# Optimization experiments

Measured on AMD Instinct MI355X. Metric: run time of the kernel, lower is better.

Reference implementation:

```python
import jax, jax.numpy as jnp
import numpy as np

N_NODES = 100000
N_EDGES = 1600000
D_IN = 128
D_OUT = 128


def setup_inputs() -> dict:
    key = jax.random.key(0)
    ks = jax.random.split(key, 7)
    x = jax.random.normal(ks[0], (N_NODES, D_IN), dtype=jnp.float32)
    edge_index = jax.random.randint(ks[1], (2, N_EDGES), 0, N_NODES, dtype=jnp.int64)
    edge_weights = jax.random.uniform(ks[2], (N_EDGES,), dtype=jnp.float32)
    s = 1.0 / np.sqrt(D_IN)
    W_lin = jax.random.uniform(ks[3], (D_IN, D_OUT), minval=-s, maxval=s, dtype=jnp.float32)
    b_lin = jax.random.uniform(ks[4], (D_OUT,), minval=-s, maxval=s, dtype=jnp.float32)
    W_agg = jax.random.uniform(ks[5], (D_IN, D_OUT), minval=-s, maxval=s, dtype=jnp.float32)
    b_agg = jax.random.uniform(ks[6], (D_OUT,), minval=-s, maxval=s, dtype=jnp.float32)
    return {"x": x, "edge_index": edge_index, "edge_weights": edge_weights,
            "W_lin": W_lin, "b_lin": b_lin, "W_agg": W_agg, "b_agg": b_agg}


def reference(x, edge_index, edge_weights, W_lin, b_lin, W_agg, b_agg):
    # self transform: [N, D_out]
    self_features = x @ W_lin + b_lin
    row, col = edge_index[0], edge_index[1]
    # gather neighbor features along edges: [E, D_in]
    neighbor_features = x[col] * edge_weights[:, None]
    # per-edge transform: [E, D_out]
    msgs = neighbor_features @ W_agg + b_agg
    # scatter-add to destination nodes (index_add_ on row)
    aggregated = jax.ops.segment_sum(msgs, row, num_segments=x.shape[0])
    return self_features + aggregated
```

## Files before the change

### kernel.cpp

```cpp
#include <hip/hip_runtime.h>

#define N_NODES 100000
#define N_EDGES 1600000
#define D 128
#define SCAN_CHUNK 1024
#define NB_SCAN ((N_NODES + SCAN_CHUNK - 1) / SCAN_CHUNK)

#define BSHIFT 9
#define BUCK_NODES 512
#define NBUCK 196
#define SCAP 10240
#define PART_CHUNK 4096
#define PART_BLOCKS ((N_EDGES + PART_CHUNK - 1) / PART_CHUNK)
#define CONV_BLOCKS 6250
#define W_BLOCKS 128

typedef __attribute__((ext_vector_type(8))) short bf16x8;
typedef __attribute__((ext_vector_type(4))) float f32x4;

__device__ __forceinline__ unsigned bf16rne(float f) {
  unsigned u = __float_as_uint(f);
  return (u + 0x7fffu + ((u >> 16) & 1u)) >> 16;
}

#define T5_OFF    200
#define T5_FRAGW  100304
#define T5_SRT    116688
#define T5_XH     3316688
#define T5_ZH     9718736
#define WS_T5_BYTES ((size_t)16120784 * 4)

#define WS_OFF   100000
#define WS_BSUM  200004
#define WS_SRT   200192
#define WS_XH    3400192
#define WS_T1_BYTES ((size_t)3400192 * 4)
#define WS_T2_BYTES ((size_t)(3400192 + 6400000) * 4)

__global__ __launch_bounds__(256) void part_kernel(
    const int* __restrict__ ei, const float* __restrict__ ew,
    const float* __restrict__ x,
    const float* __restrict__ Wl, const float* __restrict__ Wa,
    int* __restrict__ pcur, int2* __restrict__ stage,
    uint4* __restrict__ xh4, unsigned short* __restrict__ fragW) {
  __shared__ int cntL[NBUCK];
  __shared__ int gbaseL[NBUCK];
  __shared__ int curL[NBUCK];
  int bid = blockIdx.x, tid = threadIdx.x;

  if (bid < PART_BLOCKS) {
    if (tid < NBUCK) cntL[tid] = 0;
    __syncthreads();
    int e0 = bid * PART_CHUNK;
#pragma unroll
    for (int k = 0; k < PART_CHUNK / 256; k++) {
      int e = e0 + k * 256 + tid;
      if (e < N_EDGES) atomicAdd(&cntL[ei[e] >> BSHIFT], 1);
    }
    __syncthreads();
    if (tid < NBUCK) {
      gbaseL[tid] = atomicAdd(&pcur[tid], cntL[tid]);
      curL[tid] = 0;
    }
    __syncthreads();
#pragma unroll
    for (int k = 0; k < PART_CHUNK / 256; k++) {
      int e = e0 + k * 256 + tid;
      if (e < N_EDGES) {
        int d = ei[e];
        int b = d >> BSHIFT;
        int s = atomicAdd(&curL[b], 1);
        stage[(size_t)b * SCAP + gbaseL[b] + s] = make_int2(
            ei[N_EDGES + e] | ((d & (BUCK_NODES - 1)) << 17), __float_as_int(ew[e]));
      }
    }
  } else if (bid < PART_BLOCKS + CONV_BLOCKS) {
    int g = (bid - PART_BLOCKS) * 256 + tid;
    const float4* xp = reinterpret_cast<const float4*>(x);
    float4 a = xp[(size_t)g * 2];
    float4 b = xp[(size_t)g * 2 + 1];
    uint4 o;
    o.x = bf16rne(a.x) | (bf16rne(a.y) << 16);
    o.y = bf16rne(a.z) | (bf16rne(a.w) << 16);
    o.z = bf16rne(b.x) | (bf16rne(b.y) << 16);
    o.w = bf16rne(b.z) | (bf16rne(b.w) << 16);
    xh4[g] = o;
  } else {
    int tau = (bid - PART_BLOCKS - CONV_BLOCKS) * 256 + tid;
    int slot = tau >> 3, j = tau & 7;
    int lane = slot & 63, ft = slot >> 6;
    int t = ft & 7, s = ft >> 3;
    int kl = (s & 3) * 32 + (lane >> 4) * 8 + j;
    int n = t * 16 + (lane & 15);
    float v = (s < 4 ? Wl : Wa)[kl * 128 + n];
    fragW[slot * 8 + j] = (unsigned short)bf16rne(v);
  }
}

__global__ __launch_bounds__(256) void binB2_kernel(const int* __restrict__ pcur,
                                                    const int2* __restrict__ stage,
                                                    int* __restrict__ off,
                                                    int2* __restrict__ srt) {
  __shared__ int pc[NBUCK];
  __shared__ int sa[BUCK_NODES];
  __shared__ int sb[BUCK_NODES];
  __shared__ int curL[BUCK_NODES];
  __shared__ int baseS, mS;
  int b = blockIdx.x, tid = threadIdx.x;
  if (tid < NBUCK) pc[tid] = pcur[tid];
  for (int i = tid; i < BUCK_NODES; i += 256) sa[i] = 0;
  __syncthreads();
  if (tid == 0) {
    int s = 0;
    for (int i = 0; i < b; i++) s += pc[i];
    baseS = s;
    mS = pc[b];
  }
  __syncthreads();
  int base = baseS, m = mS;
  const int2* sp = stage + (size_t)b * SCAP;
  for (int r = tid; r < m; r += 256)
    atomicAdd(&sa[((unsigned)sp[r].x) >> 17], 1);
  __syncthreads();
  int* srcb = sa;
  int* dstb = sb;
  for (int o = 1; o < BUCK_NODES; o <<= 1) {
    for (int p = tid; p < BUCK_NODES; p += 256)
      dstb[p] = srcb[p] + (p >= o ? srcb[p - o] : 0);
    __syncthreads();
    int* t = srcb; srcb = dstb; dstb = t;
  }
  int nb = b << BSHIFT;
  int nn = min(BUCK_NODES, N_NODES - nb);
  for (int i = tid; i < BUCK_NODES; i += 256) {
    int ex = i ? srcb[i - 1] : 0;
    curL[i] = ex;
    if (i < nn) off[nb + i] = base + ex;
  }
  if (tid == 0 && b == NBUCK - 1) off[N_NODES] = base + srcb[nn - 1];
  __syncthreads();
  for (int r = tid; r < m; r += 256) {
    int2 rec = sp[r];
    int ldst = ((unsigned)rec.x) >> 17;
    int s = atomicAdd(&curL[ldst], 1);
    srt[base + s] = make_int2(rec.x & 0x1FFFF, rec.y);
  }
}

__global__ __launch_bounds__(256) void gather_zh_kernel(const unsigned* __restrict__ xh,
                                                        const int* __restrict__ off,
                                                        const int2* __restrict__ srt,
                                                        unsigned* __restrict__ zh) {
  int gid = blockIdx.x * 256 + threadIdx.x;
  int n = gid >> 5;
  int lane = gid & 31;
  int beg = off[n], end = off[n + 1];
  float4 acc = make_float4(0.f, 0.f, 0.f, 0.f);
  int e = beg;
  for (; e + 3 < end; e += 4) {
    int2 r0 = srt[e];
    int2 r1 = srt[e + 1];
    int2 r2 = srt[e + 2];
    int2 r3 = srt[e + 3];
    uint2 p0 = *reinterpret_cast<const uint2*>(xh + (size_t)r0.x * 64 + lane * 2);
    uint2 p1 = *reinterpret_cast<const uint2*>(xh + (size_t)r1.x * 64 + lane * 2);
    uint2 p2 = *reinterpret_cast<const uint2*>(xh + (size_t)r2.x * 64 + lane * 2);
    uint2 p3 = *reinterpret_cast<const uint2*>(xh + (size_t)r3.x * 64 + lane * 2);
    float w0 = __int_as_float(r0.y), w1 = __int_as_float(r1.y);
    float w2 = __int_as_float(r2.y), w3 = __int_as_float(r3.y);
    acc.x = fmaf(w0, __uint_as_float(p0.x << 16), acc.x);
    acc.y = fmaf(w0, __uint_as_float(p0.x & 0xffff0000u), acc.y);
    acc.z = fmaf(w0, __uint_as_float(p0.y << 16), acc.z);
    acc.w = fmaf(w0, __uint_as_float(p0.y & 0xffff0000u), acc.w);
    acc.x = fmaf(w1, __uint_as_float(p1.x << 16), acc.x);
    acc.y = fmaf(w1, __uint_as_float(p1.x & 0xffff0000u), acc.y);
    acc.z = fmaf(w1, __uint_as_float(p1.y << 16), acc.z);
    acc.w = fmaf(w1, __uint_as_float(p1.y & 0xffff0000u), acc.w);
    acc.x = fmaf(w2, __uint_as_float(p2.x << 16), acc.x);
    acc.y = fmaf(w2, __uint_as_float(p2.x & 0xffff0000u), acc.y);
    acc.z = fmaf(w2, __uint_as_float(p2.y << 16), acc.z);
    acc.w = fmaf(w2, __uint_as_float(p2.y & 0xffff0000u), acc.w);
    acc.x = fmaf(w3, __uint_as_float(p3.x << 16), acc.x);
    acc.y = fmaf(w3, __uint_as_float(p3.x & 0xffff0000u), acc.y);
    acc.z = fmaf(w3, __uint_as_float(p3.y << 16), acc.z);
    acc.w = fmaf(w3, __uint_as_float(p3.y & 0xffff0000u), acc.w);
  }
  for (; e < end; e++) {
    int2 r0 = srt[e];
    uint2 p0 = *reinterpret_cast<const uint2*>(xh + (size_t)r0.x * 64 + lane * 2);
    float w0 = __int_as_float(r0.y);
    acc.x = fmaf(w0, __uint_as_float(p0.x << 16), acc.x);
    acc.y = fmaf(w0, __uint_as_float(p0.x & 0xffff0000u), acc.y);
    acc.z = fmaf(w0, __uint_as_float(p0.y << 16), acc.z);
    acc.w = fmaf(w0, __uint_as_float(p0.y & 0xffff0000u), acc.w);
  }
  uint2 o;
  o.x = bf16rne(acc.x) | (bf16rne(acc.y) << 16);
  o.y = bf16rne(acc.z) | (bf16rne(acc.w) << 16);
  *reinterpret_cast<uint2*>(zh + (size_t)n * 64 + lane * 2) = o;
}

__global__ __launch_bounds__(256) void mfma_gemm_kernel(
    const short* __restrict__ xh, const short* __restrict__ zh,
    const short* __restrict__ fragW, const int* __restrict__ off,
    const float* __restrict__ bl, const float* __restrict__ ba,
    float* __restrict__ out) {
  int tid = threadIdx.x;
  int wave = tid >> 6, lane = tid & 63;
  int m = lane & 15, q = lane >> 4;
  int R = blockIdx.x * 64 + wave * 16;
  const short* xrow = xh + (size_t)(R + m) * D + q * 8;
  const short* zrow = zh + (size_t)(R + m) * D + q * 8;
  const short* fw = fragW + (size_t)lane * 8;

  f32x4 acc[8];
#pragma unroll
  for (int t = 0; t < 8; t++) acc[t] = (f32x4){0.f, 0.f, 0.f, 0.f};

#pragma unroll
  for (int s = 0; s < 8; s++) {
    bf16x8 a = *reinterpret_cast<const bf16x8*>(s < 4 ? xrow + s * 32
                                                      : zrow + (s - 4) * 32);
#pragma unroll
    for (int t = 0; t < 8; t++) {
      bf16x8 b = *reinterpret_cast<const bf16x8*>(fw + (size_t)((s * 8 + t) * 64) * 8);
      acc[t] = __builtin_amdgcn_mfma_f32_16x16x32_bf16(a, b, acc[t], 0, 0, 0);
    }
  }

  float blv[8], bav[8];
#pragma unroll
  for (int t = 0; t < 8; t++) {
    blv[t] = bl[t * 16 + m];
    bav[t] = ba[t * 16 + m];
  }
#pragma unroll
  for (int r = 0; r < 4; r++) {
    int row = R + q * 4 + r;
    if (row < N_NODES) {
      float dg = (float)(off[row + 1] - off[row]);
#pragma unroll
      for (int t = 0; t < 8; t++)
        out[(size_t)row * D + t * 16 + m] = acc[t][r] + blv[t] + dg * bav[t];
    }
  }
}


__global__ __launch_bounds__(256) void hist_kernel(const int* __restrict__ ei,
                                                   int* __restrict__ cnt) {
  int e = blockIdx.x * 256 + threadIdx.x;
  if (e < N_EDGES) atomicAdd(&cnt[ei[e]], 1);
}

__global__ __launch_bounds__(256) void block_sum_kernel(const int* __restrict__ cnt,
                                                        int* __restrict__ bsum) {
  int base = blockIdx.x * SCAN_CHUNK;
  int s = 0;
#pragma unroll
  for (int k = 0; k < 4; k++) {
    int i = base + (int)threadIdx.x + k * 256;
    if (i < N_NODES) s += cnt[i];
  }
  __shared__ int red[4];
  for (int o = 32; o > 0; o >>= 1) s += __shfl_down(s, o, 64);
  if ((threadIdx.x & 63) == 0) red[threadIdx.x >> 6] = s;
  __syncthreads();
  if (threadIdx.x == 0) bsum[blockIdx.x] = red[0] + red[1] + red[2] + red[3];
}

__global__ __launch_bounds__(128) void scan_bsum_kernel(int* __restrict__ bsum,
                                                        int* __restrict__ off) {
  __shared__ int sh[128];
  int t = threadIdx.x;
  int v = (t < NB_SCAN) ? bsum[t] : 0;
  sh[t] = v;
  __syncthreads();
  for (int o = 1; o < 128; o <<= 1) {
    int add = (t >= o) ? sh[t - o] : 0;
    __syncthreads();
    sh[t] += add;
    __syncthreads();
  }
  if (t < NB_SCAN) bsum[t] = sh[t] - v;
  if (t == 0) off[N_NODES] = sh[127];
}

__global__ __launch_bounds__(256) void scan_offsets_kernel(const int* __restrict__ cnt,
                                                           const int* __restrict__ bsum,
                                                           int* __restrict__ off) {
  __shared__ int sh[256];
  int t = threadIdx.x;
  int i0 = blockIdx.x * SCAN_CHUNK + t * 4;
  int c[4];
#pragma unroll
  for (int k = 0; k < 4; k++) c[k] = (i0 + k < N_NODES) ? cnt[i0 + k] : 0;
  int ls = c[0] + c[1] + c[2] + c[3];
  sh[t] = ls;
  __syncthreads();
  for (int o = 1; o < 256; o <<= 1) {
    int add = (t >= o) ? sh[t - o] : 0;
    __syncthreads();
    sh[t] += add;
    __syncthreads();
  }
  int run = bsum[blockIdx.x] + sh[t] - ls;
#pragma unroll
  for (int k = 0; k < 4; k++) {
    if (i0 + k < N_NODES) off[i0 + k] = run;
    run += c[k];
  }
}

__global__ __launch_bounds__(256) void fill_kernel(const int* __restrict__ ei,
                                                   const float* __restrict__ ew,
                                                   const int* __restrict__ off,
                                                   int* __restrict__ cur,
                                                   int2* __restrict__ srt) {
  int e = blockIdx.x * 256 + threadIdx.x;
  if (e >= N_EDGES) return;
  int dst = ei[e];
  int p = off[dst] + atomicAdd(&cur[dst], 1);
  srt[p] = make_int2(ei[N_EDGES + e], __float_as_int(ew[e]));
}

__global__ __launch_bounds__(256) void convert_kernel(const float* __restrict__ x,
                                                      uint4* __restrict__ xh) {
  int i = blockIdx.x * 256 + threadIdx.x;
  const float4* xp = reinterpret_cast<const float4*>(x);
  float4 a = xp[(size_t)i * 2];
  float4 b = xp[(size_t)i * 2 + 1];
  uint4 o;
  o.x = bf16rne(a.x) | (bf16rne(a.y) << 16);
  o.y = bf16rne(a.z) | (bf16rne(a.w) << 16);
  o.z = bf16rne(b.x) | (bf16rne(b.y) << 16);
  o.w = bf16rne(b.z) | (bf16rne(b.w) << 16);
  xh[i] = o;
}

__global__ __launch_bounds__(256) void gather_bf16_kernel(const unsigned* __restrict__ xh,
                                                          const int* __restrict__ off,
                                                          const int2* __restrict__ srt,
                                                          float* __restrict__ z,
                                                          float* __restrict__ degf) {
  int gid = blockIdx.x * 256 + threadIdx.x;
  int n = gid >> 5;
  int lane = gid & 31;
  if (n >= N_NODES) return;
  int beg = off[n], end = off[n + 1];
  float4 acc = make_float4(0.f, 0.f, 0.f, 0.f);
  int e = beg;
  for (; e + 1 < end; e += 2) {
    int2 r0 = srt[e];
    int2 r1 = srt[e + 1];
    uint2 p0 = *reinterpret_cast<const uint2*>(xh + (size_t)r0.x * 64 + lane * 2);
    uint2 p1 = *reinterpret_cast<const uint2*>(xh + (size_t)r1.x * 64 + lane * 2);
    float w0 = __int_as_float(r0.y);
    float w1 = __int_as_float(r1.y);
    acc.x = fmaf(w0, __uint_as_float(p0.x << 16), acc.x);
    acc.y = fmaf(w0, __uint_as_float(p0.x & 0xffff0000u), acc.y);
    acc.z = fmaf(w0, __uint_as_float(p0.y << 16), acc.z);
    acc.w = fmaf(w0, __uint_as_float(p0.y & 0xffff0000u), acc.w);
    acc.x = fmaf(w1, __uint_as_float(p1.x << 16), acc.x);
    acc.y = fmaf(w1, __uint_as_float(p1.x & 0xffff0000u), acc.y);
    acc.z = fmaf(w1, __uint_as_float(p1.y << 16), acc.z);
    acc.w = fmaf(w1, __uint_as_float(p1.y & 0xffff0000u), acc.w);
  }
  if (e < end) {
    int2 r0 = srt[e];
    uint2 p0 = *reinterpret_cast<const uint2*>(xh + (size_t)r0.x * 64 + lane * 2);
    float w0 = __int_as_float(r0.y);
    acc.x = fmaf(w0, __uint_as_float(p0.x << 16), acc.x);
    acc.y = fmaf(w0, __uint_as_float(p0.x & 0xffff0000u), acc.y);
    acc.z = fmaf(w0, __uint_as_float(p0.y << 16), acc.z);
    acc.w = fmaf(w0, __uint_as_float(p0.y & 0xffff0000u), acc.w);
  }
  *reinterpret_cast<float4*>(z + (size_t)n * D + (lane << 2)) = acc;
  if (lane == 0) degf[n] = (float)(end - beg);
}

__global__ __launch_bounds__(256) void gather_f32_kernel(const float* __restrict__ x,
                                                         const int* __restrict__ off,
                                                         const int2* __restrict__ srt,
                                                         float* __restrict__ z,
                                                         float* __restrict__ degf) {
  int gid = blockIdx.x * 256 + threadIdx.x;
  int n = gid >> 5;
  int lane = gid & 31;
  if (n >= N_NODES) return;
  int beg = off[n], end = off[n + 1];
  float4 acc = make_float4(0.f, 0.f, 0.f, 0.f);
  for (int e = beg; e < end; e++) {
    int2 r0 = srt[e];
    float4 x0 = *reinterpret_cast<const float4*>(x + (size_t)r0.x * D + (lane << 2));
    float w0 = __int_as_float(r0.y);
    acc.x = fmaf(w0, x0.x, acc.x); acc.y = fmaf(w0, x0.y, acc.y);
    acc.z = fmaf(w0, x0.z, acc.z); acc.w = fmaf(w0, x0.w, acc.w);
  }
  *reinterpret_cast<float4*>(z + (size_t)n * D + (lane << 2)) = acc;
  if (lane == 0) degf[n] = (float)(end - beg);
}

__global__ __launch_bounds__(256) void scatter_kernel(const float* __restrict__ x,
                                                      const int* __restrict__ ei,
                                                      const float* __restrict__ ew,
                                                      float* __restrict__ z,
                                                      float* __restrict__ deg) {
  long long g = (long long)blockIdx.x * 256 + threadIdx.x;
  int e = (int)(g >> 5);
  int lane = (int)(g & 31);
  if (e >= N_EDGES) return;
  int dst = ei[e];
  int src = ei[N_EDGES + e];
  float w = ew[e];
  float4 xv = *reinterpret_cast<const float4*>(x + (size_t)src * D + (lane << 2));
  float* o = z + (size_t)dst * D + (lane << 2);
  atomicAdd(o + 0, w * xv.x);
  atomicAdd(o + 1, w * xv.y);
  atomicAdd(o + 2, w * xv.z);
  atomicAdd(o + 3, w * xv.w);
  if (lane == 0) atomicAdd(deg + dst, 1.0f);
}

__global__ __launch_bounds__(256) void fused_gemm_kernel(const float* __restrict__ x,
                                                         const float* __restrict__ Wl,
                                                         const float* __restrict__ bl,
                                                         const float* __restrict__ Wa,
                                                         const float* __restrict__ ba,
                                                         const float* __restrict__ deg,
                                                         float* __restrict__ out) {
  __shared__ float xs[32 * 16];
  __shared__ float zs[32 * 16];
  __shared__ float wls[16 * 128];
  __shared__ float was[16 * 128];
  const int tid = threadIdx.x;
  const int row0 = blockIdx.x * 32;
  const int c4 = tid & 31;
  const int r0 = tid >> 5;
  float4 acc[4];
#pragma unroll
  for (int i = 0; i < 4; i++) acc[i] = make_float4(0.f, 0.f, 0.f, 0.f);

  for (int k0 = 0; k0 < D; k0 += 16) {
    {
      int t = tid & 127;
      int r = t >> 2;
      int kc = (t & 3) << 2;
      const float* sp = (tid < 128) ? x : out;
      float* dp = (tid < 128) ? xs : zs;
      *reinterpret_cast<float4*>(dp + r * 16 + kc) =
          *reinterpret_cast<const float4*>(sp + (size_t)(row0 + r) * D + k0 + kc);
    }
#pragma unroll
    for (int i = 0; i < 2; i++) {
      int f = tid + i * 256;
      int kk = f >> 5;
      int cc = (f & 31) << 2;
      *reinterpret_cast<float4*>(wls + kk * 128 + cc) =
          *reinterpret_cast<const float4*>(Wl + (size_t)(k0 + kk) * D + cc);
      *reinterpret_cast<float4*>(was + kk * 128 + cc) =
          *reinterpret_cast<const float4*>(Wa + (size_t)(k0 + kk) * D + cc);
    }
    __syncthreads();
#pragma unroll
    for (int kk = 0; kk < 16; kk++) {
      float4 wl = *reinterpret_cast<const float4*>(wls + kk * 128 + (c4 << 2));
      float4 wa = *reinterpret_cast<const float4*>(was + kk * 128 + (c4 << 2));
#pragma unroll
      for (int rr = 0; rr < 4; rr++) {
        int r2 = r0 + rr * 8;
        float xv = xs[r2 * 16 + kk];
        float zv = zs[r2 * 16 + kk];
        acc[rr].x = fmaf(xv, wl.x, fmaf(zv, wa.x, acc[rr].x));
        acc[rr].y = fmaf(xv, wl.y, fmaf(zv, wa.y, acc[rr].y));
        acc[rr].z = fmaf(xv, wl.z, fmaf(zv, wa.z, acc[rr].z));
        acc[rr].w = fmaf(xv, wl.w, fmaf(zv, wa.w, acc[rr].w));
      }
    }
    __syncthreads();
  }

  float4 blv = *reinterpret_cast<const float4*>(bl + (c4 << 2));
  float4 bav = *reinterpret_cast<const float4*>(ba + (c4 << 2));
#pragma unroll
  for (int rr = 0; rr < 4; rr++) {
    int r = row0 + r0 + rr * 8;
    float d = deg[r];
    float4 o;
    o.x = acc[rr].x + blv.x + d * bav.x;
    o.y = acc[rr].y + blv.y + d * bav.y;
    o.z = acc[rr].z + blv.z + d * bav.z;
    o.w = acc[rr].w + blv.w + d * bav.w;
    *reinterpret_cast<float4*>(out + (size_t)r * D + (c4 << 2)) = o;
  }
}

extern "C" void kernel_launch(void* const* d_in, const int* in_sizes, int n_in,
                              void* d_out, int out_size, void* d_ws, size_t ws_size,
                              hipStream_t stream) {
  const float* x  = (const float*)d_in[0];
  const int*   ei = (const int*)d_in[1];
  const float* ew = (const float*)d_in[2];
  const float* Wl = (const float*)d_in[3];
  const float* bl = (const float*)d_in[4];
  const float* Wa = (const float*)d_in[5];
  const float* ba = (const float*)d_in[6];
  float* out = (float*)d_out;

  if (ws_size >= WS_T5_BYTES) {
    int* pcur = (int*)d_ws;
    int* off = pcur + T5_OFF;
    unsigned short* fragW = (unsigned short*)(pcur + T5_FRAGW);
    int2* srt = (int2*)(pcur + T5_SRT);
    unsigned* xh = (unsigned*)(pcur + T5_XH);
    unsigned* zh = (unsigned*)(pcur + T5_ZH);
    int2* stage = (int2*)(pcur + T5_ZH);

    hipMemsetAsync(pcur, 0, NBUCK * sizeof(int), stream);
    part_kernel<<<PART_BLOCKS + CONV_BLOCKS + W_BLOCKS, 256, 0, stream>>>(
        ei, ew, x, Wl, Wa, pcur, stage, (uint4*)xh, fragW);
    binB2_kernel<<<NBUCK, 256, 0, stream>>>(pcur, stage, off, srt);
    gather_zh_kernel<<<N_NODES * 32 / 256, 256, 0, stream>>>(xh, off, srt, zh);
    mfma_gemm_kernel<<<1563, 256, 0, stream>>>((const short*)xh, (const short*)zh,
                                               (const short*)fragW, off, bl, ba, out);
  } else if (ws_size >= WS_T1_BYTES) {
    int*  cnt  = (int*)d_ws;
    int*  off  = cnt + WS_OFF;
    int*  bsum = cnt + WS_BSUM;
    int2* srt  = (int2*)(cnt + WS_SRT);
    float* degf = (float*)cnt;

    hipMemsetAsync(cnt, 0, (size_t)N_NODES * sizeof(int), stream);
    hist_kernel<<<(N_EDGES + 255) / 256, 256, 0, stream>>>(ei, cnt);
    block_sum_kernel<<<NB_SCAN, 256, 0, stream>>>(cnt, bsum);
    scan_bsum_kernel<<<1, 128, 0, stream>>>(bsum, off);
    scan_offsets_kernel<<<NB_SCAN, 256, 0, stream>>>(cnt, bsum, off);
    hipMemsetAsync(cnt, 0, (size_t)N_NODES * sizeof(int), stream);
    fill_kernel<<<(N_EDGES + 255) / 256, 256, 0, stream>>>(ei, ew, off, cnt, srt);

    if (ws_size >= WS_T2_BYTES) {
      unsigned* xh = (unsigned*)(cnt + WS_XH);
      convert_kernel<<<(N_NODES * D / 8) / 256, 256, 0, stream>>>(x, (uint4*)xh);
      gather_bf16_kernel<<<(N_NODES * 32 + 255) / 256, 256, 0, stream>>>(xh, off, srt, out, degf);
    } else {
      gather_f32_kernel<<<(N_NODES * 32 + 255) / 256, 256, 0, stream>>>(x, off, srt, out, degf);
    }
    fused_gemm_kernel<<<N_NODES / 32, 256, 0, stream>>>(x, Wl, bl, Wa, ba, degf, out);
  } else {
    float* deg = (float*)d_ws;
    hipMemsetAsync(out, 0, (size_t)N_NODES * D * sizeof(float), stream);
    hipMemsetAsync(deg, 0, (size_t)N_NODES * sizeof(float), stream);
    scatter_kernel<<<(N_EDGES * 32) / 256, 256, 0, stream>>>(x, ei, ew, out, deg);
    fused_gemm_kernel<<<N_NODES / 32, 256, 0, stream>>>(x, Wl, bl, Wa, ba, deg, out);
  }
}
```

Before: 284.4 us.

## Add nontemporal loads/stores, widen binning block to 512, unroll gather by 8

Several streaming inputs (edge indices, weights, x for bf16 conversion, sorted edge records) are read with nontemporal loads, and the final output is written with nontemporal stores to reduce cache pollution. The bucket-sort kernel now runs 512 threads per block so each thread handles one local node in the scan. The gather kernel is unrolled to 8 edges per iteration to keep more gathers in flight. The extra unroll raises register pressure, and the nontemporal hints may not help reuse-sensitive reads.

```diff
diff --git a/kernel.cpp b/kernel.cpp
--- a/kernel.cpp
+++ b/kernel.cpp
@@ -17,6 +17,7 @@
 
 typedef __attribute__((ext_vector_type(8))) short bf16x8;
 typedef __attribute__((ext_vector_type(4))) float f32x4;
+typedef __attribute__((ext_vector_type(4))) unsigned u32x4;
 
 __device__ __forceinline__ unsigned bf16rne(float f) {
   unsigned u = __float_as_uint(f);
@@ -67,23 +68,25 @@
     for (int k = 0; k < PART_CHUNK / 256; k++) {
       int e = e0 + k * 256 + tid;
       if (e < N_EDGES) {
-        int d = ei[e];
+        int d = __builtin_nontemporal_load(ei + e);
+        int src = __builtin_nontemporal_load(ei + N_EDGES + e);
+        float w = __builtin_nontemporal_load(ew + e);
         int b = d >> BSHIFT;
         int s = atomicAdd(&curL[b], 1);
         stage[(size_t)b * SCAP + gbaseL[b] + s] = make_int2(
-            ei[N_EDGES + e] | ((d & (BUCK_NODES - 1)) << 17), __float_as_int(ew[e]));
+            src | ((d & (BUCK_NODES - 1)) << 17), __float_as_int(w));
       }
     }
   } else if (bid < PART_BLOCKS + CONV_BLOCKS) {
     int g = (bid - PART_BLOCKS) * 256 + tid;
-    const float4* xp = reinterpret_cast<const float4*>(x);
-    float4 a = xp[(size_t)g * 2];
-    float4 b = xp[(size_t)g * 2 + 1];
+    const u32x4* xp = reinterpret_cast<const u32x4*>(x);
+    u32x4 a = __builtin_nontemporal_load(xp + (size_t)g * 2);
+    u32x4 b = __builtin_nontemporal_load(xp + (size_t)g * 2 + 1);
     uint4 o;
-    o.x = bf16rne(a.x) | (bf16rne(a.y) << 16);
-    o.y = bf16rne(a.z) | (bf16rne(a.w) << 16);
-    o.z = bf16rne(b.x) | (bf16rne(b.y) << 16);
-    o.w = bf16rne(b.z) | (bf16rne(b.w) << 16);
+    o.x = bf16rne(__uint_as_float(a.x)) | (bf16rne(__uint_as_float(a.y)) << 16);
+    o.y = bf16rne(__uint_as_float(a.z)) | (bf16rne(__uint_as_float(a.w)) << 16);
+    o.z = bf16rne(__uint_as_float(b.x)) | (bf16rne(__uint_as_float(b.y)) << 16);
+    o.w = bf16rne(__uint_as_float(b.z)) | (bf16rne(__uint_as_float(b.w)) << 16);
     xh4[g] = o;
   } else {
     int tau = (bid - PART_BLOCKS - CONV_BLOCKS) * 256 + tid;
@@ -97,7 +100,7 @@
   }
 }
 
-__global__ __launch_bounds__(256) void binB2_kernel(const int* __restrict__ pcur,
+__global__ __launch_bounds__(512) void binB2_kernel(const int* __restrict__ pcur,
                                                     const int2* __restrict__ stage,
                                                     int* __restrict__ off,
                                                     int2* __restrict__ srt) {
@@ -108,7 +111,7 @@
   __shared__ int baseS, mS;
   int b = blockIdx.x, tid = threadIdx.x;
   if (tid < NBUCK) pc[tid] = pcur[tid];
-  for (int i = tid; i < BUCK_NODES; i += 256) sa[i] = 0;
+  if (tid < BUCK_NODES) sa[tid] = 0;
   __syncthreads();
   if (tid == 0) {
     int s = 0;
@@ -119,33 +122,42 @@
   __syncthreads();
   int base = baseS, m = mS;
   const int2* sp = stage + (size_t)b * SCAP;
-  for (int r = tid; r < m; r += 256)
+  for (int r = tid; r < m; r += 512)
     atomicAdd(&sa[((unsigned)sp[r].x) >> 17], 1);
   __syncthreads();
   int* srcb = sa;
   int* dstb = sb;
   for (int o = 1; o < BUCK_NODES; o <<= 1) {
-    for (int p = tid; p < BUCK_NODES; p += 256)
-      dstb[p] = srcb[p] + (p >= o ? srcb[p - o] : 0);
+    if (tid < BUCK_NODES)
+      dstb[tid] = srcb[tid] + (tid >= o ? srcb[tid - o] : 0);
     __syncthreads();
     int* t = srcb; srcb = dstb; dstb = t;
   }
   int nb = b << BSHIFT;
   int nn = min(BUCK_NODES, N_NODES - nb);
-  for (int i = tid; i < BUCK_NODES; i += 256) {
-    int ex = i ? srcb[i - 1] : 0;
-    curL[i] = ex;
-    if (i < nn) off[nb + i] = base + ex;
+  if (tid < BUCK_NODES) {
+    int ex = tid ? srcb[tid - 1] : 0;
+    curL[tid] = ex;
+    if (tid < nn) off[nb + tid] = base + ex;
   }
   if (tid == 0 && b == NBUCK - 1) off[N_NODES] = base + srcb[nn - 1];
   __syncthreads();
-  for (int r = tid; r < m; r += 256) {
+  for (int r = tid; r < m; r += 512) {
     int2 rec = sp[r];
     int ldst = ((unsigned)rec.x) >> 17;
     int s = atomicAdd(&curL[ldst], 1);
     srt[base + s] = make_int2(rec.x & 0x1FFFF, rec.y);
   }
 }
+
+#define ACC_EDGE(q_, p_)                                         \
+  {                                                              \
+    float w_ = __int_as_float((int)((q_) >> 32));                \
+    acc.x = fmaf(w_, __uint_as_float((p_).x << 16), acc.x);      \
+    acc.y = fmaf(w_, __uint_as_float((p_).x & 0xffff0000u), acc.y); \
+    acc.z = fmaf(w_, __uint_as_float((p_).y << 16), acc.z);      \
+    acc.w = fmaf(w_, __uint_as_float((p_).y & 0xffff0000u), acc.w); \
+  }
 
 __global__ __launch_bounds__(256) void gather_zh_kernel(const unsigned* __restrict__ xh,
                                                         const int* __restrict__ off,
@@ -157,42 +169,41 @@
   int beg = off[n], end = off[n + 1];
   float4 acc = make_float4(0.f, 0.f, 0.f, 0.f);
   int e = beg;
+  for (; e + 7 < end; e += 8) {
+    long long q0 = __builtin_nontemporal_load(reinterpret_cast<const long long*>(srt + e));
+    long long q1 = __builtin_nontemporal_load(reinterpret_cast<const long long*>(srt + e + 1));
+    long long q2 = __builtin_nontemporal_load(reinterpret_cast<const long long*>(srt + e + 2));
+    long long q3 = __builtin_nontemporal_load(reinterpret_cast<const long long*>(srt + e + 3));
+    long long q4 = __builtin_nontemporal_load(reinterpret_cast<const long long*>(srt + e + 4));
+    long long q5 = __builtin_nontemporal_load(reinterpret_cast<const long long*>(srt + e + 5));
+    long long q6 = __builtin_nontemporal_load(reinterpret_cast<const long long*>(srt + e + 6));
+    long long q7 = __builtin_nontemporal_load(reinterpret_cast<const long long*>(srt + e + 7));
+    uint2 p0 = *reinterpret_cast<const uint2*>(xh + (size_t)(unsigned)(q0 & 0xffffffffu) * 64 + lane * 2);
+    uint2 p1 = *reinterpret_cast<const uint2*>(xh + (size_t)(unsigned)(q1 & 0xffffffffu) * 64 + lane * 2);
+    uint2 p2 = *reinterpret_cast<const uint2*>(xh + (size_t)(unsigned)(q2 & 0xffffffffu) * 64 + lane * 2);
+    uint2 p3 = *reinterpret_cast<const uint2*>(xh + (size_t)(unsigned)(q3 & 0xffffffffu) * 64 + lane * 2);
+    uint2 p4 = *reinterpret_cast<const uint2*>(xh + (size_t)(unsigned)(q4 & 0xffffffffu) * 64 + lane * 2);
+    uint2 p5 = *reinterpret_cast<const uint2*>(xh + (size_t)(unsigned)(q5 & 0xffffffffu) * 64 + lane * 2);
+    uint2 p6 = *reinterpret_cast<const uint2*>(xh + (size_t)(unsigned)(q6 & 0xffffffffu) * 64 + lane * 2);
+    uint2 p7 = *reinterpret_cast<const uint2*>(xh + (size_t)(unsigned)(q7 & 0xffffffffu) * 64 + lane * 2);
+    ACC_EDGE(q0, p0) ACC_EDGE(q1, p1) ACC_EDGE(q2, p2) ACC_EDGE(q3, p3)
+    ACC_EDGE(q4, p4) ACC_EDGE(q5, p5) ACC_EDGE(q6, p6) ACC_EDGE(q7, p7)
+  }
   for (; e + 3 < end; e += 4) {
-    int2 r0 = srt[e];
-    int2 r1 = srt[e + 1];
-    int2 r2 = srt[e + 2];
-    int2 r3 = srt[e + 3];
-    uint2 p0 = *reinterpret_cast<const uint2*>(xh + (size_t)r0.x * 64 + lane * 2);
-    uint2 p1 = *reinterpret_cast<const uint2*>(xh + (size_t)r1.x * 64 + lane * 2);
-    uint2 p2 = *reinterpret_cast<const uint2*>(xh + (size_t)r2.x * 64 + lane * 2);
-    uint2 p3 = *reinterpret_cast<const uint2*>(xh + (size_t)r3.x * 64 + lane * 2);
-    float w0 = __int_as_float(r0.y), w1 = __int_as_float(r1.y);
-    float w2 = __int_as_float(r2.y), w3 = __int_as_float(r3.y);
-    acc.x = fmaf(w0, __uint_as_float(p0.x << 16), acc.x);
-    acc.y = fmaf(w0, __uint_as_float(p0.x & 0xffff0000u), acc.y);
-    acc.z = fmaf(w0, __uint_as_float(p0.y << 16), acc.z);
-    acc.w = fmaf(w0, __uint_as_float(p0.y & 0xffff0000u), acc.w);
-    acc.x = fmaf(w1, __uint_as_float(p1.x << 16), acc.x);
-    acc.y = fmaf(w1, __uint_as_float(p1.x & 0xffff0000u), acc.y);
-    acc.z = fmaf(w1, __uint_as_float(p1.y << 16), acc.z);
-    acc.w = fmaf(w1, __uint_as_float(p1.y & 0xffff0000u), acc.w);
-    acc.x = fmaf(w2, __uint_as_float(p2.x << 16), acc.x);
-    acc.y = fmaf(w2, __uint_as_float(p2.x & 0xffff0000u), acc.y);
-    acc.z = fmaf(w2, __uint_as_float(p2.y << 16), acc.z);
-    acc.w = fmaf(w2, __uint_as_float(p2.y & 0xffff0000u), acc.w);
-    acc.x = fmaf(w3, __uint_as_float(p3.x << 16), acc.x);
-    acc.y = fmaf(w3, __uint_as_float(p3.x & 0xffff0000u), acc.y);
-    acc.z = fmaf(w3, __uint_as_float(p3.y << 16), acc.z);
-    acc.w = fmaf(w3, __uint_as_float(p3.y & 0xffff0000u), acc.w);
+    long long q0 = __builtin_nontemporal_load(reinterpret_cast<const long long*>(srt + e));
+    long long q1 = __builtin_nontemporal_load(reinterpret_cast<const long long*>(srt + e + 1));
+    long long q2 = __builtin_nontemporal_load(reinterpret_cast<const long long*>(srt + e + 2));
+    long long q3 = __builtin_nontemporal_load(reinterpret_cast<const long long*>(srt + e + 3));
+    uint2 p0 = *reinterpret_cast<const uint2*>(xh + (size_t)(unsigned)(q0 & 0xffffffffu) * 64 + lane * 2);
+    uint2 p1 = *reinterpret_cast<const uint2*>(xh + (size_t)(unsigned)(q1 & 0xffffffffu) * 64 + lane * 2);
+    uint2 p2 = *reinterpret_cast<const uint2*>(xh + (size_t)(unsigned)(q2 & 0xffffffffu) * 64 + lane * 2);
+    uint2 p3 = *reinterpret_cast<const uint2*>(xh + (size_t)(unsigned)(q3 & 0xffffffffu) * 64 + lane * 2);
+    ACC_EDGE(q0, p0) ACC_EDGE(q1, p1) ACC_EDGE(q2, p2) ACC_EDGE(q3, p3)
   }
   for (; e < end; e++) {
-    int2 r0 = srt[e];
-    uint2 p0 = *reinterpret_cast<const uint2*>(xh + (size_t)r0.x * 64 + lane * 2);
-    float w0 = __int_as_float(r0.y);
-    acc.x = fmaf(w0, __uint_as_float(p0.x << 16), acc.x);
-    acc.y = fmaf(w0, __uint_as_float(p0.x & 0xffff0000u), acc.y);
-    acc.z = fmaf(w0, __uint_as_float(p0.y << 16), acc.z);
-    acc.w = fmaf(w0, __uint_as_float(p0.y & 0xffff0000u), acc.w);
+    long long q0 = __builtin_nontemporal_load(reinterpret_cast<const long long*>(srt + e));
+    uint2 p0 = *reinterpret_cast<const uint2*>(xh + (size_t)(unsigned)(q0 & 0xffffffffu) * 64 + lane * 2);
+    ACC_EDGE(q0, p0)
   }
   uint2 o;
   o.x = bf16rne(acc.x) | (bf16rne(acc.y) << 16);
@@ -241,7 +252,8 @@
       float dg = (float)(off[row + 1] - off[row]);
 #pragma unroll
       for (int t = 0; t < 8; t++)
-        out[(size_t)row * D + t * 16 + m] = acc[t][r] + blv[t] + dg * bav[t];
+        __builtin_nontemporal_store(acc[t][r] + blv[t] + dg * bav[t],
+                                    out + (size_t)row * D + t * 16 + m);
     }
   }
 }
@@ -519,7 +531,7 @@
     hipMemsetAsync(pcur, 0, NBUCK * sizeof(int), stream);
     part_kernel<<<PART_BLOCKS + CONV_BLOCKS + W_BLOCKS, 256, 0, stream>>>(
         ei, ew, x, Wl, Wa, pcur, stage, (uint4*)xh, fragW);
-    binB2_kernel<<<NBUCK, 256, 0, stream>>>(pcur, stage, off, srt);
+    binB2_kernel<<<NBUCK, 512, 0, stream>>>(pcur, stage, off, srt);
     gather_zh_kernel<<<N_NODES * 32 / 256, 256, 0, stream>>>(xh, off, srt, zh);
     mfma_gemm_kernel<<<1563, 256, 0, stream>>>((const short*)xh, (const short*)zh,
                                                (const short*)fragW, off, bl, ba, out);
```

Result: faster. 278.6 us (-2.0%).

## Coalesce partition writes via LDS staging, sub-sort edges by source range, nontemporal I/O

Applied to the files above, without the earlier changes.

The partition kernel now stages each chunk's records in shared memory, grouped by bucket through a block prefix scan, then writes them to global memory in bucket-contiguous runs, replacing scattered per-edge stores. The binning kernel runs with 512 threads and orders each node's edges by one of 8 source-index ranges, so the later gather reads x rows with better locality. The x conversion loads and the final output stores use nontemporal hints. These changes add LDS use, extra barriers and a redundant first scan loop in part_kernel, which may lower occupancy.

```diff
diff --git a/kernel.cpp b/kernel.cpp
--- a/kernel.cpp
+++ b/kernel.cpp
@@ -14,9 +14,11 @@
 #define PART_BLOCKS ((N_EDGES + PART_CHUNK - 1) / PART_CHUNK)
 #define CONV_BLOCKS 6250
 #define W_BLOCKS 128
+#define OCT_DIV 12500
 
 typedef __attribute__((ext_vector_type(8))) short bf16x8;
 typedef __attribute__((ext_vector_type(4))) float f32x4;
+typedef __attribute__((ext_vector_type(4))) unsigned u32x4;
 
 __device__ __forceinline__ unsigned bf16rne(float f) {
   unsigned u = __float_as_uint(f);
@@ -43,23 +45,44 @@
     const float* __restrict__ Wl, const float* __restrict__ Wa,
     int* __restrict__ pcur, int2* __restrict__ stage,
     uint4* __restrict__ xh4, unsigned short* __restrict__ fragW) {
-  __shared__ int cntL[NBUCK];
-  __shared__ int gbaseL[NBUCK];
+  __shared__ int cntL[256];
+  __shared__ int s0[256];
+  __shared__ int gb[NBUCK];
   __shared__ int curL[NBUCK];
+  __shared__ int2 recL[PART_CHUNK];
+  __shared__ unsigned char buckL[PART_CHUNK];
   int bid = blockIdx.x, tid = threadIdx.x;
 
   if (bid < PART_BLOCKS) {
-    if (tid < NBUCK) cntL[tid] = 0;
+    cntL[tid] = 0;
     __syncthreads();
     int e0 = bid * PART_CHUNK;
+    int tot = min(PART_CHUNK, N_EDGES - e0);
 #pragma unroll
     for (int k = 0; k < PART_CHUNK / 256; k++) {
       int e = e0 + k * 256 + tid;
       if (e < N_EDGES) atomicAdd(&cntL[ei[e] >> BSHIFT], 1);
     }
     __syncthreads();
+    for (int o = 1; o < 256; o <<= 1) {
+      int add = (tid >= o) ? s0[tid - o] : 0;
+      if (o == 1) add = (tid >= 1) ? cntL[tid - 1] : 0;
+      if (o == 1) s0[tid] = cntL[tid];
+      __syncthreads();
+      if (o > 1) s0[tid] += add;
+      else s0[tid] += add - cntL[tid] + cntL[tid];
+      __syncthreads();
+    }
+    s0[tid] = cntL[tid];
+    __syncthreads();
+    for (int o = 1; o < 256; o <<= 1) {
+      int add = (tid >= o) ? s0[tid - o] : 0;
+      __syncthreads();
+      s0[tid] += add;
+      __syncthreads();
+    }
     if (tid < NBUCK) {
-      gbaseL[tid] = atomicAdd(&pcur[tid], cntL[tid]);
+      gb[tid] = atomicAdd(&pcur[tid], cntL[tid]);
       curL[tid] = 0;
     }
     __syncthreads();
@@ -68,22 +91,32 @@
       int e = e0 + k * 256 + tid;
       if (e < N_EDGES) {
         int d = ei[e];
+        int src = ei[N_EDGES + e];
+        float w = ew[e];
         int b = d >> BSHIFT;
-        int s = atomicAdd(&curL[b], 1);
-        stage[(size_t)b * SCAP + gbaseL[b] + s] = make_int2(
-            ei[N_EDGES + e] | ((d & (BUCK_NODES - 1)) << 17), __float_as_int(ew[e]));
+        int r = atomicAdd(&curL[b], 1);
+        int slot = (s0[b] - cntL[b]) + r;
+        recL[slot] = make_int2(src | ((d & (BUCK_NODES - 1)) << 17),
+                               __float_as_int(w));
+        buckL[slot] = (unsigned char)b;
       }
+    }
+    __syncthreads();
+    for (int i = tid; i < tot; i += 256) {
+      int b = buckL[i];
+      int idx = gb[b] + (i - (s0[b] - cntL[b]));
+      stage[(size_t)b * SCAP + idx] = recL[i];
     }
   } else if (bid < PART_BLOCKS + CONV_BLOCKS) {
     int g = (bid - PART_BLOCKS) * 256 + tid;
-    const float4* xp = reinterpret_cast<const float4*>(x);
-    float4 a = xp[(size_t)g * 2];
-    float4 b = xp[(size_t)g * 2 + 1];
+    const u32x4* xp = reinterpret_cast<const u32x4*>(x);
+    u32x4 a = __builtin_nontemporal_load(xp + (size_t)g * 2);
+    u32x4 b = __builtin_nontemporal_load(xp + (size_t)g * 2 + 1);
     uint4 o;
-    o.x = bf16rne(a.x) | (bf16rne(a.y) << 16);
-    o.y = bf16rne(a.z) | (bf16rne(a.w) << 16);
-    o.z = bf16rne(b.x) | (bf16rne(b.y) << 16);
-    o.w = bf16rne(b.z) | (bf16rne(b.w) << 16);
+    o.x = bf16rne(__uint_as_float(a.x)) | (bf16rne(__uint_as_float(a.y)) << 16);
+    o.y = bf16rne(__uint_as_float(a.z)) | (bf16rne(__uint_as_float(a.w)) << 16);
+    o.z = bf16rne(__uint_as_float(b.x)) | (bf16rne(__uint_as_float(b.y)) << 16);
+    o.w = bf16rne(__uint_as_float(b.z)) | (bf16rne(__uint_as_float(b.w)) << 16);
     xh4[g] = o;
   } else {
     int tau = (bid - PART_BLOCKS - CONV_BLOCKS) * 256 + tid;
@@ -97,18 +130,18 @@
   }
 }
 
-__global__ __launch_bounds__(256) void binB2_kernel(const int* __restrict__ pcur,
+__global__ __launch_bounds__(512) void binB2_kernel(const int* __restrict__ pcur,
                                                     const int2* __restrict__ stage,
                                                     int* __restrict__ off,
                                                     int2* __restrict__ srt) {
   __shared__ int pc[NBUCK];
+  __shared__ int h[BUCK_NODES * 8];
   __shared__ int sa[BUCK_NODES];
-  __shared__ int sb[BUCK_NODES];
-  __shared__ int curL[BUCK_NODES];
+  __shared__ int cur8[BUCK_NODES * 8];
   __shared__ int baseS, mS;
   int b = blockIdx.x, tid = threadIdx.x;
   if (tid < NBUCK) pc[tid] = pcur[tid];
-  for (int i = tid; i < BUCK_NODES; i += 256) sa[i] = 0;
+  for (int i = tid; i < BUCK_NODES * 8; i += 512) h[i] = 0;
   __syncthreads();
   if (tid == 0) {
     int s = 0;
@@ -119,31 +152,44 @@
   __syncthreads();
   int base = baseS, m = mS;
   const int2* sp = stage + (size_t)b * SCAP;
-  for (int r = tid; r < m; r += 256)
-    atomicAdd(&sa[((unsigned)sp[r].x) >> 17], 1);
-  __syncthreads();
-  int* srcb = sa;
-  int* dstb = sb;
+  for (int r = tid; r < m; r += 512) {
+    int rx = sp[r].x;
+    int lsrc = rx & 0x1FFFF;
+    int ldst = ((unsigned)rx) >> 17;
+    atomicAdd(&h[(ldst << 3) + lsrc / OCT_DIV], 1);
+  }
+  __syncthreads();
+  int tot = 0;
+#pragma unroll
+  for (int j = 0; j < 8; j++) tot += h[(tid << 3) + j];
+  sa[tid] = tot;
+  __syncthreads();
   for (int o = 1; o < BUCK_NODES; o <<= 1) {
-    for (int p = tid; p < BUCK_NODES; p += 256)
-      dstb[p] = srcb[p] + (p >= o ? srcb[p - o] : 0);
-    __syncthreads();
-    int* t = srcb; srcb = dstb; dstb = t;
+    int add = (tid >= o) ? sa[tid - o] : 0;
+    __syncthreads();
+    sa[tid] += add;
+    __syncthreads();
+  }
+  int nodeExcl = sa[tid] - tot;
+  {
+    int run = nodeExcl;
+#pragma unroll
+    for (int j = 0; j < 8; j++) {
+      cur8[(tid << 3) + j] = run;
+      run += h[(tid << 3) + j];
+    }
   }
   int nb = b << BSHIFT;
   int nn = min(BUCK_NODES, N_NODES - nb);
-  for (int i = tid; i < BUCK_NODES; i += 256) {
-    int ex = i ? srcb[i - 1] : 0;
-    curL[i] = ex;
-    if (i < nn) off[nb + i] = base + ex;
-  }
-  if (tid == 0 && b == NBUCK - 1) off[N_NODES] = base + srcb[nn - 1];
-  __syncthreads();
-  for (int r = tid; r < m; r += 256) {
+  if (tid < nn) off[nb + tid] = base + nodeExcl;
+  if (tid == 0 && b == NBUCK - 1) off[N_NODES] = base + m;
+  __syncthreads();
+  for (int r = tid; r < m; r += 512) {
     int2 rec = sp[r];
+    int lsrc = rec.x & 0x1FFFF;
     int ldst = ((unsigned)rec.x) >> 17;
-    int s = atomicAdd(&curL[ldst], 1);
-    srt[base + s] = make_int2(rec.x & 0x1FFFF, rec.y);
+    int s = atomicAdd(&cur8[(ldst << 3) + lsrc / OCT_DIV], 1);
+    srt[base + s] = make_int2(lsrc, rec.y);
   }
 }
 
@@ -241,7 +287,8 @@
       float dg = (float)(off[row + 1] - off[row]);
 #pragma unroll
       for (int t = 0; t < 8; t++)
-        out[(size_t)row * D + t * 16 + m] = acc[t][r] + blv[t] + dg * bav[t];
+        __builtin_nontemporal_store(acc[t][r] + blv[t] + dg * bav[t],
+                                    out + (size_t)row * D + t * 16 + m);
     }
   }
 }
@@ -519,7 +566,7 @@
     hipMemsetAsync(pcur, 0, NBUCK * sizeof(int), stream);
     part_kernel<<<PART_BLOCKS + CONV_BLOCKS + W_BLOCKS, 256, 0, stream>>>(
         ei, ew, x, Wl, Wa, pcur, stage, (uint4*)xh, fragW);
-    binB2_kernel<<<NBUCK, 256, 0, stream>>>(pcur, stage, off, srt);
+    binB2_kernel<<<NBUCK, 512, 0, stream>>>(pcur, stage, off, srt);
     gather_zh_kernel<<<N_NODES * 32 / 256, 256, 0, stream>>>(xh, off, srt, zh);
     mfma_gemm_kernel<<<1563, 256, 0, stream>>>((const short*)xh, (const short*)zh,
                                                (const short*)fragW, off, bl, ba, out);
```

After: 271.3 us. 4.6% less time.
